# Kernel tuning notes

Measured on AMD Instinct MI355X. Metric: run time of the kernel, lower is better.

The kernel has to match this reference:

```python
import jax, jax.numpy as jnp
import numpy as np

N_NODES = 50000
N_EDGES = 65536
D_NODE = 1024
D_HID = 1024


def setup_inputs() -> dict:
    key = jax.random.key(0)
    k1, k2, k3, k4, k5 = jax.random.split(key, 5)
    node_feats = jax.random.normal(k1, (N_NODES, D_NODE), dtype=jnp.float32)
    src = jax.random.randint(k2, (N_EDGES,), 0, N_NODES, dtype=jnp.int64)
    dst = jax.random.randint(k3, (N_EDGES,), 0, N_NODES, dtype=jnp.int64)
    # MLP([2048, 1024, 1024]) with ReLU between layers, bias, no BN, no dropout
    W1 = jax.random.normal(k4, (2 * D_NODE, D_HID), dtype=jnp.float32) * (1.0 / np.sqrt(2 * D_NODE))
    b1 = jnp.zeros((D_HID,), dtype=jnp.float32)
    W2 = jax.random.normal(k5, (D_HID, D_HID), dtype=jnp.float32) * (1.0 / np.sqrt(D_HID))
    b2 = jnp.zeros((D_HID,), dtype=jnp.float32)
    return {"node_feats": node_feats, "src": src, "dst": dst,
            "W1": W1, "b1": b1, "W2": W2, "b2": b2}


def reference(node_feats, src, dst, W1, b1, W2, b2):
    # gather per-edge src/dst node features and concat: [E, 2d]
    feat = jnp.concatenate([node_feats[src], node_feats[dst]], axis=1)
    # edge MLP: Linear -> ReLU -> Linear
    h = jax.nn.relu(feat @ W1 + b1)
    e_f = h @ W2 + b2  # [E, D_HID]
    return e_f
```

## Files before the change

kernel.cpp:

```cpp
#include <hip/hip_runtime.h>
#include <stdint.h>
#include <stddef.h>

typedef unsigned short u16;
typedef __bf16 bf16_t;
typedef bf16_t bf16x8 __attribute__((ext_vector_type(8)));
typedef float f32x4 __attribute__((ext_vector_type(4)));
typedef u16 u16x4 __attribute__((ext_vector_type(4)));

#define N_NODES 50000
#define N_EDGES 65536
#define D_NODE 1024
#define D_HID 1024

#define BM 256
#define BK 64
#define BUFE (BM * BK)
#define LDS_BYTES (4 * BUFE * 2)


__device__ __forceinline__ u16 f2bf(float f) {
  union { float f; uint32_t u; } v; v.f = f;
  uint32_t u = v.u;
  u += 0x7FFF + ((u >> 16) & 1);
  return (u16)(u >> 16);
}

typedef __attribute__((address_space(1))) const void GV;
typedef __attribute__((address_space(3))) void LV;

__device__ __forceinline__ void gll16(const void* g, void* lds_wave_base) {
  __builtin_amdgcn_global_load_lds((GV*)g, (LV*)lds_wave_base, 16, 0, 0);
}


__global__ void detect_i64_kernel(const int* __restrict__ src, int* __restrict__ flag) {
  if (threadIdx.x == 0 && blockIdx.x == 0) {
    int o = 0;
    for (int i = 1; i < 32; i += 2) o |= src[i];
    *flag = (o == 0) ? 1 : 0;
  }
}

__global__ void cvt_bf16_kernel(const float* __restrict__ in, u16* __restrict__ out, size_t n4) {
  size_t i = (size_t)blockIdx.x * blockDim.x + threadIdx.x;
  if (i >= n4) return;
  float4 v = reinterpret_cast<const float4*>(in)[i];
  u16x4 o;
  o.x = f2bf(v.x); o.y = f2bf(v.y); o.z = f2bf(v.z); o.w = f2bf(v.w);
  reinterpret_cast<u16x4*>(out)[i] = o;
}

__global__ void transpose_cvt_kernel(const float* __restrict__ in, u16* __restrict__ out,
                                     int K, int N) {
  __shared__ float tile[32][33];
  int n0 = blockIdx.x * 32, k0 = blockIdx.y * 32;
  int tx = threadIdx.x, ty = threadIdx.y;
  #pragma unroll
  for (int i = ty; i < 32; i += 8)
    tile[i][tx] = in[(size_t)(k0 + i) * N + (n0 + tx)];
  __syncthreads();
  #pragma unroll
  for (int i = ty; i < 32; i += 8)
    out[(size_t)(n0 + i) * K + (k0 + tx)] = f2bf(tile[tx][i]);
}


template <bool FIRST>
__device__ __forceinline__ void gemm_body(const u16* __restrict__ Abf,
                                          const int* __restrict__ src,
                                          const int* __restrict__ dst,
                                          const int* __restrict__ is64p,
                                          const u16* __restrict__ Bt,
                                          const float* __restrict__ bias,
                                          u16* __restrict__ hout,
                                          float* __restrict__ fout,
                                          const int K) {
  extern __shared__ __align__(16) u16 lds[];
  u16* const ldsA = lds;
  u16* const ldsB = lds + 2 * BUFE;

  const int t = threadIdx.x;
  const int lane = t & 63;
  const int wave = t >> 6;

  const int b = blockIdx.x;
  const int wgid = (b & 7) * 128 + (b >> 3);
  const int bm = (wgid >> 2) * BM;
  const int bn = (wgid & 3) * BM;

  const int wm = (wave >> 1) * 128;
  const int wn = (wave & 1) * 128;

  const int srb = t >> 3;
  const int kswz = (((t & 7) ^ (srb & 7)) << 3);

  uint32_t aoff[8], doff[8], boff[8];
  if constexpr (FIRST) {
    const int is64 = *is64p;
    #pragma unroll
    for (int qr = 0; qr < 8; ++qr) {
      const int row = qr * 32 + srb;
      const int e = bm + row;
      const int s = is64 ? src[2 * e] : src[e];
      const int d = is64 ? dst[2 * e] : dst[e];
      aoff[qr] = ((uint32_t)s * D_NODE + (uint32_t)kswz) * 2u;
      doff[qr] = ((uint32_t)d * D_NODE + (uint32_t)kswz) * 2u;
      boff[qr] = ((uint32_t)(bn + row) * (uint32_t)K + (uint32_t)kswz) * 2u;
    }
  } else {
    #pragma unroll
    for (int qr = 0; qr < 8; ++qr) {
      const int row = qr * 32 + srb;
      aoff[qr] = ((uint32_t)(bm + row) * (uint32_t)K + (uint32_t)kswz) * 2u;
      boff[qr] = ((uint32_t)(bn + row) * (uint32_t)K + (uint32_t)kswz) * 2u;
    }
  }

  auto stageA = [&](int buf, int qr, int u) {
    uint32_t off;
    if constexpr (FIRST) {
      off = (u < D_NODE / BK) ? aoff[qr] + (uint32_t)(u * BK * 2)
                              : doff[qr] + (uint32_t)((u - D_NODE / BK) * BK * 2);
    } else {
      off = aoff[qr] + (uint32_t)(u * BK * 2);
    }
    gll16((const char*)Abf + off, ldsA + buf * BUFE + qr * 2048 + wave * 512);
  };
  auto stageB = [&](int buf, int qr, int u) {
    gll16((const char*)Bt + (boff[qr] + (uint32_t)(u * BK * 2)),
          ldsB + buf * BUFE + qr * 2048 + wave * 512);
  };
  auto stageGroup = [&](int buf, int u) {
    #pragma unroll
    for (int qr = 0; qr < 8; ++qr) stageA(buf, qr, u);
    #pragma unroll
    for (int qr = 0; qr < 8; ++qr) stageB(buf, qr, u);
  };

  const int lm = lane & 15;
  const int qw = lane >> 4;
  const int kq8 = qw << 3;
  const int swzr = (lm & 7) << 3;
  const int kb0 = kq8 ^ swzr;
  const int kb1 = (32 + kq8) ^ swzr;
  const int arow = (wm + lm) * BK;
  const int brow = (wn + lm) * BK;

  f32x4 acc[8][8] = {};

  const int NT = K / BK;

  stageGroup(0, 0);
  __syncthreads();

  for (int u = 0; u < NT; ++u) {
    const int cb = u & 1;
    const u16* As_c = ldsA + cb * BUFE;
    const u16* Bs_c = ldsB + cb * BUFE;

    if (u + 1 < NT) stageGroup(cb ^ 1, u + 1);

    bf16x8 bf0[8];
    #pragma unroll
    for (int j = 0; j < 8; ++j)
      bf0[j] = *reinterpret_cast<const bf16x8*>(Bs_c + brow + j * 1024 + kb0);
    #pragma unroll
    for (int i = 0; i < 8; ++i) {
      bf16x8 a = *reinterpret_cast<const bf16x8*>(As_c + arow + i * 1024 + kb0);
      #pragma unroll
      for (int j = 0; j < 8; ++j)
        acc[i][j] = __builtin_amdgcn_mfma_f32_16x16x32_bf16(a, bf0[j], acc[i][j], 0, 0, 0);
    }

    bf16x8 bf1[8];
    #pragma unroll
    for (int j = 0; j < 8; ++j)
      bf1[j] = *reinterpret_cast<const bf16x8*>(Bs_c + brow + j * 1024 + kb1);
    #pragma unroll
    for (int i = 0; i < 8; ++i) {
      bf16x8 a = *reinterpret_cast<const bf16x8*>(As_c + arow + i * 1024 + kb1);
      #pragma unroll
      for (int j = 0; j < 8; ++j)
        acc[i][j] = __builtin_amdgcn_mfma_f32_16x16x32_bf16(a, bf1[j], acc[i][j], 0, 0, 0);
    }

    __syncthreads();
  }

  const int rq = qw * 4;
  #pragma unroll
  for (int j = 0; j < 8; ++j) {
    const int n = bn + wn + 16 * j + lm;
    const float bj = bias[n];
    #pragma unroll
    for (int i = 0; i < 8; ++i) {
      const int m0 = bm + wm + 16 * i + rq;
      f32x4 c = acc[i][j];
      #pragma unroll
      for (int rr = 0; rr < 4; ++rr) {
        float vv = c[rr] + bj;
        if (FIRST) {
          vv = fmaxf(vv, 0.0f);
          hout[(size_t)(m0 + rr) * D_HID + n] = f2bf(vv);
        } else {
          fout[(size_t)(m0 + rr) * D_HID + n] = vv;
        }
      }
    }
  }
}

__launch_bounds__(256, 1)
__global__ void gemm1_kernel(const u16* __restrict__ Abf, const int* __restrict__ src,
                             const int* __restrict__ dst, const int* __restrict__ is64p,
                             const u16* __restrict__ Bt, const float* __restrict__ bias,
                             u16* __restrict__ hout) {
  gemm_body<true>(Abf, src, dst, is64p, Bt, bias, hout, nullptr, 2 * D_NODE);
}

__launch_bounds__(256, 1)
__global__ void gemm2_kernel(const u16* __restrict__ Abf, const u16* __restrict__ Bt,
                             const float* __restrict__ bias, float* __restrict__ fout) {
  gemm_body<false>(Abf, nullptr, nullptr, nullptr, Bt, bias, nullptr, fout, D_HID);
}


extern "C" void kernel_launch(void* const* d_in, const int* in_sizes, int n_in,
                              void* d_out, int out_size, void* d_ws, size_t ws_size,
                              hipStream_t stream) {
  const float* node_feats = (const float*)d_in[0];
  const int*   src        = (const int*)d_in[1];
  const int*   dst        = (const int*)d_in[2];
  const float* W1         = (const float*)d_in[3];
  const float* b1         = (const float*)d_in[4];
  const float* W2         = (const float*)d_in[5];
  const float* b2         = (const float*)d_in[6];
  float* out = (float*)d_out;

  u16* ws = (u16*)d_ws;
  const size_t NODE_E = (size_t)N_NODES * D_NODE;
  u16* node_bf = ws;
  u16* W1T = node_bf + NODE_E;
  u16* W2T = W1T + (size_t)2048 * 1024;
  u16* h   = W2T + (size_t)1024 * 1024;
  int* flag = (int*)(h + (size_t)N_EDGES * D_HID);

  static bool attr_set = false;
  if (!attr_set) {
    hipFuncSetAttribute(reinterpret_cast<const void*>(&gemm1_kernel),
                        hipFuncAttributeMaxDynamicSharedMemorySize, LDS_BYTES);
    hipFuncSetAttribute(reinterpret_cast<const void*>(&gemm2_kernel),
                        hipFuncAttributeMaxDynamicSharedMemorySize, LDS_BYTES);
    attr_set = true;
  }

  detect_i64_kernel<<<1, 64, 0, stream>>>(src, flag);

  cvt_bf16_kernel<<<(unsigned)(NODE_E / 4 / 256), 256, 0, stream>>>(node_feats, node_bf, NODE_E / 4);

  transpose_cvt_kernel<<<dim3(1024 / 32, 2048 / 32), dim3(32, 8), 0, stream>>>(W1, W1T, 2048, 1024);
  transpose_cvt_kernel<<<dim3(1024 / 32, 1024 / 32), dim3(32, 8), 0, stream>>>(W2, W2T, 1024, 1024);

  gemm1_kernel<<<1024, 256, LDS_BYTES, stream>>>(node_bf, src, dst, flag, W1T, b1, h);

  gemm2_kernel<<<1024, 256, LDS_BYTES, stream>>>(h, W2T, b2, out);
}
```

Before: 993.9 us.

## Retile GEMMs to 256x128x32 with static LDS, two blocks per CU

Shrinks the block tile from 256x256 with BK=64 to 256x128 with BK=32. LDS moves to static shared arrays, which drops the dynamic-size attribute setup. The smaller per-block LDS and accumulator footprint lets two workgroups run per CU (launch_bounds 256,2) with twice as many blocks. The tile is staged in a new two-rows-per-chunk swizzled layout, and the MFMA loop is wrapped in s_setprio. The aim is more latency hiding through occupancy. The cost is lower per-block reuse, more global loads per flop, and more barriers per K step.

Measured after the change: 886.9 us. 10.8% less time.

```diff
diff --git a/kernel.cpp b/kernel.cpp
--- a/kernel.cpp
+++ b/kernel.cpp
@@ -14,9 +14,10 @@
 #define D_HID 1024
 
 #define BM 256
-#define BK 64
-#define BUFE (BM * BK)
-#define LDS_BYTES (4 * BUFE * 2)
+#define BN 128
+#define BK 32
+#define ABUFE (BM * BK)
+#define BBUFE (BN * BK)
 
 
 __device__ __forceinline__ u16 f2bf(float f) {
@@ -76,121 +77,115 @@
                                           u16* __restrict__ hout,
                                           float* __restrict__ fout,
                                           const int K) {
-  extern __shared__ __align__(16) u16 lds[];
-  u16* const ldsA = lds;
-  u16* const ldsB = lds + 2 * BUFE;
+  __shared__ __align__(16) u16 ldsA[2][ABUFE];
+  __shared__ __align__(16) u16 ldsB[2][BBUFE];
 
   const int t = threadIdx.x;
   const int lane = t & 63;
   const int wave = t >> 6;
 
   const int b = blockIdx.x;
-  const int wgid = (b & 7) * 128 + (b >> 3);
-  const int bm = (wgid >> 2) * BM;
-  const int bn = (wgid & 3) * BM;
+  const int wgid = (b & 7) * 256 + (b >> 3);
+  const int bm = (wgid >> 3) * BM;
+  const int bn = (wgid & 7) * BN;
 
   const int wm = (wave >> 1) * 128;
-  const int wn = (wave & 1) * 128;
-
-  const int srb = t >> 3;
-  const int kswz = (((t & 7) ^ (srb & 7)) << 3);
-
-  uint32_t aoff[8], doff[8], boff[8];
+  const int wn = (wave & 1) * 64;
+
+  const int v = (t & 7) ^ ((t >> 3) & 7);
+  const int crow = 2 * (t >> 3) + (v >> 2);
+  const uint32_t koff = (uint32_t)(v & 3) * 16u;
+
+  uint32_t aoff[4], doff[4] = {0, 0, 0, 0}, boff[2];
   if constexpr (FIRST) {
     const int is64 = *is64p;
     #pragma unroll
-    for (int qr = 0; qr < 8; ++qr) {
-      const int row = qr * 32 + srb;
-      const int e = bm + row;
+    for (int q = 0; q < 4; ++q) {
+      const int e = bm + crow + q * 64;
       const int s = is64 ? src[2 * e] : src[e];
       const int d = is64 ? dst[2 * e] : dst[e];
-      aoff[qr] = ((uint32_t)s * D_NODE + (uint32_t)kswz) * 2u;
-      doff[qr] = ((uint32_t)d * D_NODE + (uint32_t)kswz) * 2u;
-      boff[qr] = ((uint32_t)(bn + row) * (uint32_t)K + (uint32_t)kswz) * 2u;
+      aoff[q] = (uint32_t)s * (D_NODE * 2u) + koff;
+      doff[q] = (uint32_t)d * (D_NODE * 2u) + koff;
     }
   } else {
     #pragma unroll
-    for (int qr = 0; qr < 8; ++qr) {
-      const int row = qr * 32 + srb;
-      aoff[qr] = ((uint32_t)(bm + row) * (uint32_t)K + (uint32_t)kswz) * 2u;
-      boff[qr] = ((uint32_t)(bn + row) * (uint32_t)K + (uint32_t)kswz) * 2u;
+    for (int q = 0; q < 4; ++q)
+      aoff[q] = (uint32_t)(bm + crow + q * 64) * (uint32_t)(K * 2) + koff;
+  }
+  #pragma unroll
+  for (int q = 0; q < 2; ++q)
+    boff[q] = (uint32_t)(bn + crow + q * 64) * (uint32_t)(K * 2) + koff;
+
+  const int ldst = wave * 512;
+
+  auto stage = [&](int buf, int u) {
+    if constexpr (FIRST) {
+      uint32_t ka;
+      if (u < D_NODE / BK) {
+        ka = (uint32_t)(u * BK * 2);
+        gll16((const char*)Abf + (aoff[0] + ka), &ldsA[buf][ldst]);
+        gll16((const char*)Abf + (aoff[1] + ka), &ldsA[buf][2048 + ldst]);
+        gll16((const char*)Abf + (aoff[2] + ka), &ldsA[buf][4096 + ldst]);
+        gll16((const char*)Abf + (aoff[3] + ka), &ldsA[buf][6144 + ldst]);
+      } else {
+        ka = (uint32_t)((u - D_NODE / BK) * BK * 2);
+        gll16((const char*)Abf + (doff[0] + ka), &ldsA[buf][ldst]);
+        gll16((const char*)Abf + (doff[1] + ka), &ldsA[buf][2048 + ldst]);
+        gll16((const char*)Abf + (doff[2] + ka), &ldsA[buf][4096 + ldst]);
+        gll16((const char*)Abf + (doff[3] + ka), &ldsA[buf][6144 + ldst]);
+      }
+    } else {
+      const uint32_t ka = (uint32_t)(u * BK * 2);
+      gll16((const char*)Abf + (aoff[0] + ka), &ldsA[buf][ldst]);
+      gll16((const char*)Abf + (aoff[1] + ka), &ldsA[buf][2048 + ldst]);
+      gll16((const char*)Abf + (aoff[2] + ka), &ldsA[buf][4096 + ldst]);
+      gll16((const char*)Abf + (aoff[3] + ka), &ldsA[buf][6144 + ldst]);
     }
-  }
-
-  auto stageA = [&](int buf, int qr, int u) {
-    uint32_t off;
-    if constexpr (FIRST) {
-      off = (u < D_NODE / BK) ? aoff[qr] + (uint32_t)(u * BK * 2)
-                              : doff[qr] + (uint32_t)((u - D_NODE / BK) * BK * 2);
-    } else {
-      off = aoff[qr] + (uint32_t)(u * BK * 2);
-    }
-    gll16((const char*)Abf + off, ldsA + buf * BUFE + qr * 2048 + wave * 512);
-  };
-  auto stageB = [&](int buf, int qr, int u) {
-    gll16((const char*)Bt + (boff[qr] + (uint32_t)(u * BK * 2)),
-          ldsB + buf * BUFE + qr * 2048 + wave * 512);
-  };
-  auto stageGroup = [&](int buf, int u) {
-    #pragma unroll
-    for (int qr = 0; qr < 8; ++qr) stageA(buf, qr, u);
-    #pragma unroll
-    for (int qr = 0; qr < 8; ++qr) stageB(buf, qr, u);
+    const uint32_t kb = (uint32_t)(u * BK * 2);
+    gll16((const char*)Bt + (boff[0] + kb), &ldsB[buf][ldst]);
+    gll16((const char*)Bt + (boff[1] + kb), &ldsB[buf][2048 + ldst]);
   };
 
   const int lm = lane & 15;
   const int qw = lane >> 4;
-  const int kq8 = qw << 3;
-  const int swzr = (lm & 7) << 3;
-  const int kb0 = kq8 ^ swzr;
-  const int kb1 = (32 + kq8) ^ swzr;
-  const int arow = (wm + lm) * BK;
-  const int brow = (wn + lm) * BK;
-
-  f32x4 acc[8][8] = {};
+  const int slot = ((((lm & 1) << 2) | qw) ^ (lm >> 1)) * 8;
+  const int a_base = (wm / 2 + (lm >> 1)) * 64 + slot;
+  const int b_base = (wn / 2 + (lm >> 1)) * 64 + slot;
+
+  f32x4 acc[8][4] = {};
 
   const int NT = K / BK;
 
-  stageGroup(0, 0);
+  stage(0, 0);
   __syncthreads();
 
   for (int u = 0; u < NT; ++u) {
     const int cb = u & 1;
-    const u16* As_c = ldsA + cb * BUFE;
-    const u16* Bs_c = ldsB + cb * BUFE;
-
-    if (u + 1 < NT) stageGroup(cb ^ 1, u + 1);
-
-    bf16x8 bf0[8];
-    #pragma unroll
-    for (int j = 0; j < 8; ++j)
-      bf0[j] = *reinterpret_cast<const bf16x8*>(Bs_c + brow + j * 1024 + kb0);
-    #pragma unroll
-    for (int i = 0; i < 8; ++i) {
-      bf16x8 a = *reinterpret_cast<const bf16x8*>(As_c + arow + i * 1024 + kb0);
+
+    if (u + 1 < NT) stage(cb ^ 1, u + 1);
+
+    bf16x8 bfr[4], afr[8];
+    #pragma unroll
+    for (int j = 0; j < 4; ++j)
+      bfr[j] = *reinterpret_cast<const bf16x8*>(&ldsB[cb][b_base + j * 512]);
+    #pragma unroll
+    for (int i = 0; i < 8; ++i)
+      afr[i] = *reinterpret_cast<const bf16x8*>(&ldsA[cb][a_base + i * 512]);
+
+    __builtin_amdgcn_s_setprio(1);
+    #pragma unroll
+    for (int i = 0; i < 8; ++i)
       #pragma unroll
-      for (int j = 0; j < 8; ++j)
-        acc[i][j] = __builtin_amdgcn_mfma_f32_16x16x32_bf16(a, bf0[j], acc[i][j], 0, 0, 0);
-    }
-
-    bf16x8 bf1[8];
-    #pragma unroll
-    for (int j = 0; j < 8; ++j)
-      bf1[j] = *reinterpret_cast<const bf16x8*>(Bs_c + brow + j * 1024 + kb1);
-    #pragma unroll
-    for (int i = 0; i < 8; ++i) {
-      bf16x8 a = *reinterpret_cast<const bf16x8*>(As_c + arow + i * 1024 + kb1);
-      #pragma unroll
-      for (int j = 0; j < 8; ++j)
-        acc[i][j] = __builtin_amdgcn_mfma_f32_16x16x32_bf16(a, bf1[j], acc[i][j], 0, 0, 0);
-    }
+      for (int j = 0; j < 4; ++j)
+        acc[i][j] = __builtin_amdgcn_mfma_f32_16x16x32_bf16(afr[i], bfr[j], acc[i][j], 0, 0, 0);
+    __builtin_amdgcn_s_setprio(0);
 
     __syncthreads();
   }
 
   const int rq = qw * 4;
   #pragma unroll
-  for (int j = 0; j < 8; ++j) {
+  for (int j = 0; j < 4; ++j) {
     const int n = bn + wn + 16 * j + lm;
     const float bj = bias[n];
     #pragma unroll
@@ -211,7 +206,7 @@
   }
 }
 
-__launch_bounds__(256, 1)
+__launch_bounds__(256, 2)
 __global__ void gemm1_kernel(const u16* __restrict__ Abf, const int* __restrict__ src,
                              const int* __restrict__ dst, const int* __restrict__ is64p,
                              const u16* __restrict__ Bt, const float* __restrict__ bias,
@@ -219,7 +214,7 @@
   gemm_body<true>(Abf, src, dst, is64p, Bt, bias, hout, nullptr, 2 * D_NODE);
 }
 
-__launch_bounds__(256, 1)
+__launch_bounds__(256, 2)
 __global__ void gemm2_kernel(const u16* __restrict__ Abf, const u16* __restrict__ Bt,
                              const float* __restrict__ bias, float* __restrict__ fout) {
   gemm_body<false>(Abf, nullptr, nullptr, nullptr, Bt, bias, nullptr, fout, D_HID);
@@ -246,15 +241,6 @@
   u16* h   = W2T + (size_t)1024 * 1024;
   int* flag = (int*)(h + (size_t)N_EDGES * D_HID);
 
-  static bool attr_set = false;
-  if (!attr_set) {
-    hipFuncSetAttribute(reinterpret_cast<const void*>(&gemm1_kernel),
-                        hipFuncAttributeMaxDynamicSharedMemorySize, LDS_BYTES);
-    hipFuncSetAttribute(reinterpret_cast<const void*>(&gemm2_kernel),
-                        hipFuncAttributeMaxDynamicSharedMemorySize, LDS_BYTES);
-    attr_set = true;
-  }
-
   detect_i64_kernel<<<1, 64, 0, stream>>>(src, flag);
 
   cvt_bf16_kernel<<<(unsigned)(NODE_E / 4 / 256), 256, 0, stream>>>(node_feats, node_bf, NODE_E / 4);
@@ -262,7 +248,7 @@
   transpose_cvt_kernel<<<dim3(1024 / 32, 2048 / 32), dim3(32, 8), 0, stream>>>(W1, W1T, 2048, 1024);
   transpose_cvt_kernel<<<dim3(1024 / 32, 1024 / 32), dim3(32, 8), 0, stream>>>(W2, W2T, 1024, 1024);
 
-  gemm1_kernel<<<1024, 256, LDS_BYTES, stream>>>(node_bf, src, dst, flag, W1T, b1, h);
-
-  gemm2_kernel<<<1024, 256, LDS_BYTES, stream>>>(h, W2T, b2, out);
-}
+  gemm1_kernel<<<2048, 256, 0, stream>>>(node_bf, src, dst, flag, W1T, b1, h);
+
+  gemm2_kernel<<<2048, 256, 0, stream>>>(h, W2T, b2, out);
+}
```
